# Optimization experiments

Measured on AMD Instinct MI355X. Metric: run time of the kernel, lower is better.

## Reference

```python
import jax, jax.numpy as jnp
import numpy as np

N_NODES = 100000
N_EDGES = 300000
D = 128
HID = 128

def setup_inputs() -> dict:
    key = jax.random.key(0)
    ks = jax.random.split(key, 12)
    s = lambda fan_in: 1.0 / np.sqrt(fan_in)
    return {
        "user_emb": jax.random.normal(ks[0], (N_NODES, D), jnp.float32),
        "item_emb": jax.random.normal(ks[1], (N_NODES, D), jnp.float32),
        "ei_ui": jax.random.randint(ks[2], (2, N_EDGES), 0, N_NODES, jnp.int64),
        "ei_iu": jax.random.randint(ks[3], (2, N_EDGES), 0, N_NODES, jnp.int64),
        "W_bi_ui": jax.random.normal(ks[4], (2 * D, HID), jnp.float32) * s(2 * D),
        "b_bi_ui": jnp.zeros((HID,), jnp.float32),
        "W1_ui": jax.random.normal(ks[5], (HID, HID), jnp.float32) * s(HID),
        "b1_ui": jnp.zeros((HID,), jnp.float32),
        "W2_ui": jax.random.normal(ks[6], (HID, 1), jnp.float32) * s(HID),
        "b2_ui": jnp.zeros((1,), jnp.float32),
        "W_bi_iu": jax.random.normal(ks[7], (2 * D, HID), jnp.float32) * s(2 * D),
        "b_bi_iu": jnp.zeros((HID,), jnp.float32),
        "W1_iu": jax.random.normal(ks[8], (HID, HID), jnp.float32) * s(HID),
        "b1_iu": jnp.zeros((HID,), jnp.float32),
        "W2_iu": jax.random.normal(ks[9], (HID, 1), jnp.float32) * s(HID),
        "b2_iu": jnp.zeros((1,), jnp.float32),
    }

def _decode_edge_type(src_emb, dst_emb, edge_index, W_bi, b_bi, W1, b1, W2, b2):
    # gather endpoint embeddings and concat -> [E, 2D]
    e = jnp.concatenate([src_emb[edge_index[0]], dst_emb[edge_index[1]]], axis=1)
    h = jax.nn.elu(e @ W_bi + b_bi)          # bilinear -> ELU
    h = jax.nn.elu(h @ W1 + b1)              # linear1 -> ELU
    p = jax.nn.sigmoid(h @ W2 + b2)          # linear2 -> sigmoid
    return p.reshape(-1)                     # [E]

def reference(user_emb, item_emb, ei_ui, ei_iu,
              W_bi_ui, b_bi_ui, W1_ui, b1_ui, W2_ui, b2_ui,
              W_bi_iu, b_bi_iu, W1_iu, b1_iu, W2_iu, b2_iu):
    # edge type (user, clicks, item): source=user, target=item
    p_ui = _decode_edge_type(user_emb, item_emb, ei_ui,
                             W_bi_ui, b_bi_ui, W1_ui, b1_ui, W2_ui, b2_ui)
    # edge type (item, clicked_by, user): source=item, target=user
    p_iu = _decode_edge_type(item_emb, user_emb, ei_iu,
                             W_bi_iu, b_bi_iu, W1_iu, b1_iu, W2_iu, b2_iu)
    return jnp.stack([p_ui, p_iu])  # [2, E]
```

## Files before the change

kernel.cpp:

```cpp
#include <hip/hip_runtime.h>

typedef __attribute__((ext_vector_type(8))) short short8;
typedef __attribute__((ext_vector_type(4))) float float4v;
typedef __attribute__((ext_vector_type(4))) int int4v;

#define E_EDGES 300000
#define EPB 128
#define NBLK ((E_EDGES + EPB - 1) / EPB)
#define TAB_ELEMS 12800000

__device__ __forceinline__ short f2bf(float f) {
    unsigned u = __float_as_uint(f);
    return (short)((u + 0x7FFFu + ((u >> 16) & 1u)) >> 16);
}
__device__ __forceinline__ unsigned pk_bf16(float a, float b) {
    unsigned ua = __float_as_uint(a), ub = __float_as_uint(b);
    ua += 0x7FFFu + ((ua >> 16) & 1u);
    ub += 0x7FFFu + ((ub >> 16) & 1u);
    return __builtin_amdgcn_perm(ub, ua, 0x07060302);
}
__device__ __forceinline__ void cp16(const void* g, void* l) {
    __builtin_amdgcn_global_load_lds(
        (const __attribute__((address_space(1))) unsigned int*)g,
        (__attribute__((address_space(3))) unsigned int*)l, 16, 0, 0);
}

__global__ void prep_all(const float* __restrict__ ue, const float* __restrict__ ie,
                         const float* __restrict__ Wbi_ui, const float* __restrict__ W1_ui,
                         const float* __restrict__ Wbi_iu, const float* __restrict__ W1_iu,
                         short* __restrict__ ws) {
    __shared__ short tr[64 * 68];
    const int t = blockIdx.y;
    const int tid = threadIdx.x;
    if (blockIdx.x < 1024) {
        const float* src = t ? ie : ue;
        short* dst = ws + 98304 + (size_t)t * TAB_ELEMS;
        const int stride = 1024 * 256;
        for (int g = blockIdx.x * 256 + tid; g < TAB_ELEMS / 8; g += stride) {
            const float* p = src + (size_t)g * 8;
            float4v v0 = ((const float4v*)p)[0];
            float4v v1 = ((const float4v*)p)[1];
            int4v w = { (int)pk_bf16(v0[0], v0[1]), (int)pk_bf16(v0[2], v0[3]),
                        (int)pk_bf16(v1[0], v1[1]), (int)pk_bf16(v1[2], v1[3]) };
            *(int4v*)(dst + (size_t)g * 8) = w;
        }
        return;
    }
    const int m = blockIdx.x - 1024;
    const float* W; int k0, n0, obase;
    if (m < 8) {
        int kt = m >> 1, nh = m & 1;
        W = t ? Wbi_iu : Wbi_ui; k0 = kt * 64; n0 = nh * 64;
        obase = t * 32768 + kt * 8192;
    } else {
        int mm = m - 8; int kt = mm >> 1, nh = mm & 1;
        W = t ? W1_iu : W1_ui; k0 = kt * 64; n0 = nh * 64;
        obase = 65536 + t * 16384 + kt * 8192;
    }
    for (int it = 0; it < 16; ++it) {
        int flat = it * 256 + tid;
        int kk = flat >> 6, nn = flat & 63;
        tr[nn * 68 + kk] = f2bf(W[(size_t)(k0 + kk) * 128 + n0 + nn]);
    }
    __syncthreads();
    for (int it = 0; it < 16; ++it) {
        int flat = it * 256 + tid;
        int nn = flat >> 6, kk = flat & 63;
        int n = n0 + nn;
        ws[obase + n * 64 + (kk ^ ((n & 7) << 3))] = tr[nn * 68 + kk];
    }
}

template<bool BF16G>
__launch_bounds__(256, 4)
__global__ void edge_decoder(
    const float* __restrict__ user_emb, const float* __restrict__ item_emb,
    const int* __restrict__ ei_ui, const int* __restrict__ ei_iu,
    const float* __restrict__ b_bi_ui, const float* __restrict__ b1_ui,
    const float* __restrict__ W2_ui, const float* __restrict__ b2_ui,
    const float* __restrict__ b_bi_iu, const float* __restrict__ b1_iu,
    const float* __restrict__ W2_iu, const float* __restrict__ b2_iu,
    const short* __restrict__ ws, const short* __restrict__ tab,
    float* __restrict__ out)
{
    __shared__ short Blds[128 * 64];
    __shared__ short Hlds[4 * 16 * 136];

    const int type = blockIdx.y;
    const int e0 = blockIdx.x * EPB;
    const int tid = threadIdx.x;
    const int wave = tid >> 6, lane = tid & 63;
    const int q = lane >> 4, ln = lane & 15;

    const int*   ei   = type ? ei_iu : ei_ui;
    const float* bbi  = type ? b_bi_iu : b_bi_ui;
    const float* b1v  = type ? b1_iu : b1_ui;
    const float* W2v  = type ? W2_iu : W2_ui;
    const float* b2v  = type ? b2_iu : b2_ui;
    const short* WbiT = ws + type * 32768;
    const short* W1T  = ws + 65536 + type * 16384;

    for (int c = 0; c < 4; ++c)
        cp16(WbiT + c * 2048 + tid * 8, Blds + c * 2048 + tid * 8);

    short8 a[2][8];
    if (BF16G) {
        for (int mt = 0; mt < 2; ++mt) {
            int erow = e0 + wave * 32 + mt * 16 + ln;
            int safe = (erow < E_EDGES) ? erow : 0;
            const short* sp = tab + (size_t)(type ? TAB_ELEMS : 0) + (size_t)ei[safe] * 128;
            const short* dp = tab + (size_t)(type ? 0 : TAB_ELEMS) + (size_t)ei[E_EDGES + safe] * 128;
            for (int ks = 0; ks < 4; ++ks)
                a[mt][ks] = *(const short8*)(sp + ks * 32 + q * 8);
            for (int ks = 4; ks < 8; ++ks)
                a[mt][ks] = *(const short8*)(dp + (ks - 4) * 32 + q * 8);
        }
    } else {
        const float* srcT = type ? item_emb : user_emb;
        const float* dstT = type ? user_emb : item_emb;
        for (int mt = 0; mt < 2; ++mt) {
            int erow = e0 + wave * 32 + mt * 16 + ln;
            int safe = (erow < E_EDGES) ? erow : 0;
            int si = ei[safe], di = ei[E_EDGES + safe];
            for (int ks = 0; ks < 8; ++ks) {
                const float* p = (ks < 4) ? (srcT + (size_t)si * 128 + ks * 32 + q * 8)
                                          : (dstT + (size_t)di * 128 + (ks - 4) * 32 + q * 8);
                float4v v0 = ((const float4v*)p)[0];
                float4v v1 = ((const float4v*)p)[1];
                int4v w = { (int)pk_bf16(v0[0], v0[1]), (int)pk_bf16(v0[2], v0[3]),
                            (int)pk_bf16(v1[0], v1[1]), (int)pk_bf16(v1[2], v1[3]) };
                a[mt][ks] = *(short8*)&w;
            }
        }
    }

    float4v acc[2][8];
    for (int nt = 0; nt < 8; ++nt) {
        float bb = bbi[nt * 16 + ln];
        acc[0][nt] = (float4v){bb, bb, bb, bb};
        acc[1][nt] = acc[0][nt];
    }

    const int swz = (ln & 7) << 3;

    for (int kt = 0; kt < 4; ++kt) {
        __syncthreads();
        for (int ks2 = 0; ks2 < 2; ++ks2) {
            int ka = (ks2 * 32 + q * 8) ^ swz;
            int ks = kt * 2 + ks2;
            for (int nt = 0; nt < 8; ++nt) {
                short8 bf = *(const short8*)&Blds[(nt * 16 + ln) * 64 + ka];
                acc[0][nt] = __builtin_amdgcn_mfma_f32_16x16x32_bf16(a[0][ks], bf, acc[0][nt], 0, 0, 0);
                acc[1][nt] = __builtin_amdgcn_mfma_f32_16x16x32_bf16(a[1][ks], bf, acc[1][nt], 0, 0, 0);
            }
        }
        __syncthreads();
        const short* nxt = (kt < 3) ? (WbiT + (kt + 1) * 8192) : W1T;
        for (int c = 0; c < 4; ++c)
            cp16(nxt + c * 2048 + tid * 8, Blds + c * 2048 + tid * 8);
    }

    short* Hw = Hlds + wave * (16 * 136);
    short8 a2[2][4];
    for (int mt = 0; mt < 2; ++mt) {
        for (int nt = 0; nt < 8; ++nt) {
            int col = nt * 16 + ln;
            float4v v = acc[mt][nt];
            for (int r = 0; r < 4; ++r) {
                float x = v[r];
                float h = x > 0.f ? x : (__expf(x) - 1.f);
                Hw[(q * 4 + r) * 136 + col] = f2bf(h);
            }
        }
        for (int ks = 0; ks < 4; ++ks)
            a2[mt][ks] = *(const short8*)&Hw[ln * 136 + ks * 32 + q * 8];
    }

    for (int nt = 0; nt < 8; ++nt) {
        float bb = b1v[nt * 16 + ln];
        acc[0][nt] = (float4v){bb, bb, bb, bb};
        acc[1][nt] = acc[0][nt];
    }

    for (int kt = 0; kt < 2; ++kt) {
        __syncthreads();
        for (int ks2 = 0; ks2 < 2; ++ks2) {
            int ka = (ks2 * 32 + q * 8) ^ swz;
            int ks = kt * 2 + ks2;
            for (int nt = 0; nt < 8; ++nt) {
                short8 bf = *(const short8*)&Blds[(nt * 16 + ln) * 64 + ka];
                acc[0][nt] = __builtin_amdgcn_mfma_f32_16x16x32_bf16(a2[0][ks], bf, acc[0][nt], 0, 0, 0);
                acc[1][nt] = __builtin_amdgcn_mfma_f32_16x16x32_bf16(a2[1][ks], bf, acc[1][nt], 0, 0, 0);
            }
        }
        __syncthreads();
        if (kt == 0)
            for (int c = 0; c < 4; ++c)
                cp16(W1T + 8192 + c * 2048 + tid * 8, Blds + c * 2048 + tid * 8);
    }

    for (int mt = 0; mt < 2; ++mt) {
        float s0 = 0.f, s1 = 0.f, s2 = 0.f, s3 = 0.f;
        for (int nt = 0; nt < 8; ++nt) {
            float wv = W2v[nt * 16 + ln];
            float4v v = acc[mt][nt];
            float x;
            x = v[0]; x = x > 0.f ? x : (__expf(x) - 1.f); s0 += x * wv;
            x = v[1]; x = x > 0.f ? x : (__expf(x) - 1.f); s1 += x * wv;
            x = v[2]; x = x > 0.f ? x : (__expf(x) - 1.f); s2 += x * wv;
            x = v[3]; x = x > 0.f ? x : (__expf(x) - 1.f); s3 += x * wv;
        }
        for (int off = 1; off < 16; off <<= 1) {
            s0 += __shfl_xor(s0, off);
            s1 += __shfl_xor(s1, off);
            s2 += __shfl_xor(s2, off);
            s3 += __shfl_xor(s3, off);
        }
        if (ln < 4) {
            float sv = (ln == 0) ? s0 : (ln == 1) ? s1 : (ln == 2) ? s2 : s3;
            int e = e0 + wave * 32 + mt * 16 + q * 4 + ln;
            if (e < E_EDGES) {
                float z = sv + b2v[0];
                out[type * E_EDGES + e] = 1.f / (1.f + __expf(-z));
            }
        }
    }
}

extern "C" void kernel_launch(void* const* d_in, const int* in_sizes, int n_in,
                              void* d_out, int out_size, void* d_ws, size_t ws_size,
                              hipStream_t stream) {
    const float* user_emb = (const float*)d_in[0];
    const float* item_emb = (const float*)d_in[1];
    const int*   ei_ui    = (const int*)d_in[2];
    const int*   ei_iu    = (const int*)d_in[3];
    const float* W_bi_ui  = (const float*)d_in[4];
    const float* b_bi_ui  = (const float*)d_in[5];
    const float* W1_ui    = (const float*)d_in[6];
    const float* b1_ui    = (const float*)d_in[7];
    const float* W2_ui    = (const float*)d_in[8];
    const float* b2_ui    = (const float*)d_in[9];
    const float* W_bi_iu  = (const float*)d_in[10];
    const float* b_bi_iu  = (const float*)d_in[11];
    const float* W1_iu    = (const float*)d_in[12];
    const float* b1_iu    = (const float*)d_in[13];
    const float* W2_iu    = (const float*)d_in[14];
    const float* b2_iu    = (const float*)d_in[15];
    short* ws  = (short*)d_ws;
    short* tab = ws + 98304;
    float* out = (float*)d_out;

    const size_t need = 98304u * 2u + (size_t)2 * TAB_ELEMS * 2u;

    hipLaunchKernelGGL(prep_all, dim3(1036, 2), dim3(256), 0, stream,
                       user_emb, item_emb, W_bi_ui, W1_ui, W_bi_iu, W1_iu, ws);
    if (ws_size >= need) {
        edge_decoder<true><<<dim3(NBLK, 2), dim3(256), 0, stream>>>(
            user_emb, item_emb, ei_ui, ei_iu,
            b_bi_ui, b1_ui, W2_ui, b2_ui,
            b_bi_iu, b1_iu, W2_iu, b2_iu,
            ws, tab, out);
    } else {
        edge_decoder<false><<<dim3(NBLK, 2), dim3(256), 0, stream>>>(
            user_emb, item_emb, ei_ui, ei_iu,
            b_bi_ui, b1_ui, W2_ui, b2_ui,
            b_bi_iu, b1_iu, W2_iu, b2_iu,
            ws, tab, out);
    }
}
```

Before: 272.4 us.

## Stage weights in 128-wide K chunks to halve LDS barrier rounds

Doubles the shared-memory weight tile from 64 to 128 K-columns and re-lays out the pre-transposed bf16 weights to a 128-stride swizzled format. The bilinear GEMM now runs in two staging rounds instead of four and the second GEMM in one instead of two, removing several syncthreads and cp16 reload phases. The larger LDS footprint lowers the occupancy hint from 4 to 3 blocks per CU, which may reduce latency hiding for the gather loads.

```diff
diff --git a/kernel.cpp b/kernel.cpp
--- a/kernel.cpp
+++ b/kernel.cpp
@@ -47,15 +47,17 @@
         return;
     }
     const int m = blockIdx.x - 1024;
-    const float* W; int k0, n0, obase;
+    const float* W; int k0, n0, obase, kbase;
     if (m < 8) {
         int kt = m >> 1, nh = m & 1;
         W = t ? Wbi_iu : Wbi_ui; k0 = kt * 64; n0 = nh * 64;
-        obase = t * 32768 + kt * 8192;
+        obase = t * 32768 + (kt >> 1) * 16384;
+        kbase = (kt & 1) * 64;
     } else {
         int mm = m - 8; int kt = mm >> 1, nh = mm & 1;
         W = t ? W1_iu : W1_ui; k0 = kt * 64; n0 = nh * 64;
-        obase = 65536 + t * 16384 + kt * 8192;
+        obase = 65536 + t * 16384;
+        kbase = kt * 64;
     }
     for (int it = 0; it < 16; ++it) {
         int flat = it * 256 + tid;
@@ -67,12 +69,15 @@
         int flat = it * 256 + tid;
         int nn = flat >> 6, kk = flat & 63;
         int n = n0 + nn;
-        ws[obase + n * 64 + (kk ^ ((n & 7) << 3))] = tr[nn * 68 + kk];
+        int kkst = kbase + kk;
+        int c = kkst >> 3, co = kkst & 7;
+        int p = (c & 8) | ((c ^ (n & 7)) & 7);
+        ws[obase + n * 128 + p * 8 + co] = tr[nn * 68 + kk];
     }
 }
 
 template<bool BF16G>
-__launch_bounds__(256, 4)
+__launch_bounds__(256, 3)
 __global__ void edge_decoder(
     const float* __restrict__ user_emb, const float* __restrict__ item_emb,
     const int* __restrict__ ei_ui, const int* __restrict__ ei_iu,
@@ -83,7 +88,7 @@
     const short* __restrict__ ws, const short* __restrict__ tab,
     float* __restrict__ out)
 {
-    __shared__ short Blds[128 * 64];
+    __shared__ short Blds[128 * 128];
     __shared__ short Hlds[4 * 16 * 136];
 
     const int type = blockIdx.y;
@@ -100,7 +105,7 @@
     const short* WbiT = ws + type * 32768;
     const short* W1T  = ws + 65536 + type * 16384;
 
-    for (int c = 0; c < 4; ++c)
+    for (int c = 0; c < 8; ++c)
         cp16(WbiT + c * 2048 + tid * 8, Blds + c * 2048 + tid * 8);
 
     short8 a[2][8];
@@ -141,24 +146,34 @@
         acc[1][nt] = acc[0][nt];
     }
 
-    const int swz = (ln & 7) << 3;
-
-    for (int kt = 0; kt < 4; ++kt) {
-        __syncthreads();
-        for (int ks2 = 0; ks2 < 2; ++ks2) {
-            int ka = (ks2 * 32 + q * 8) ^ swz;
-            int ks = kt * 2 + ks2;
-            for (int nt = 0; nt < 8; ++nt) {
-                short8 bf = *(const short8*)&Blds[(nt * 16 + ln) * 64 + ka];
-                acc[0][nt] = __builtin_amdgcn_mfma_f32_16x16x32_bf16(a[0][ks], bf, acc[0][nt], 0, 0, 0);
-                acc[1][nt] = __builtin_amdgcn_mfma_f32_16x16x32_bf16(a[1][ks], bf, acc[1][nt], 0, 0, 0);
-            }
-        }
-        __syncthreads();
-        const short* nxt = (kt < 3) ? (WbiT + (kt + 1) * 8192) : W1T;
-        for (int c = 0; c < 4; ++c)
-            cp16(nxt + c * 2048 + tid * 8, Blds + c * 2048 + tid * 8);
-    }
+    const int swz7 = ln & 7;
+#define KAOF(ks2) ((((((ks2) * 4 + q) & 8) | ((((ks2) * 4 + q) ^ swz7) & 7))) * 8)
+
+    __syncthreads();
+    for (int ks2 = 0; ks2 < 4; ++ks2) {
+        int ka = KAOF(ks2);
+        for (int nt = 0; nt < 8; ++nt) {
+            short8 bf = *(const short8*)&Blds[(nt * 16 + ln) * 128 + ka];
+            acc[0][nt] = __builtin_amdgcn_mfma_f32_16x16x32_bf16(a[0][ks2], bf, acc[0][nt], 0, 0, 0);
+            acc[1][nt] = __builtin_amdgcn_mfma_f32_16x16x32_bf16(a[1][ks2], bf, acc[1][nt], 0, 0, 0);
+        }
+    }
+    __syncthreads();
+    for (int c = 0; c < 8; ++c)
+        cp16(WbiT + 16384 + c * 2048 + tid * 8, Blds + c * 2048 + tid * 8);
+
+    __syncthreads();
+    for (int ks2 = 0; ks2 < 4; ++ks2) {
+        int ka = KAOF(ks2);
+        for (int nt = 0; nt < 8; ++nt) {
+            short8 bf = *(const short8*)&Blds[(nt * 16 + ln) * 128 + ka];
+            acc[0][nt] = __builtin_amdgcn_mfma_f32_16x16x32_bf16(a[0][4 + ks2], bf, acc[0][nt], 0, 0, 0);
+            acc[1][nt] = __builtin_amdgcn_mfma_f32_16x16x32_bf16(a[1][4 + ks2], bf, acc[1][nt], 0, 0, 0);
+        }
+    }
+    __syncthreads();
+    for (int c = 0; c < 8; ++c)
+        cp16(W1T + c * 2048 + tid * 8, Blds + c * 2048 + tid * 8);
 
     short* Hw = Hlds + wave * (16 * 136);
     short8 a2[2][4];
@@ -182,22 +197,16 @@
         acc[1][nt] = acc[0][nt];
     }
 
-    for (int kt = 0; kt < 2; ++kt) {
-        __syncthreads();
-        for (int ks2 = 0; ks2 < 2; ++ks2) {
-            int ka = (ks2 * 32 + q * 8) ^ swz;
-            int ks = kt * 2 + ks2;
-            for (int nt = 0; nt < 8; ++nt) {
-                short8 bf = *(const short8*)&Blds[(nt * 16 + ln) * 64 + ka];
-                acc[0][nt] = __builtin_amdgcn_mfma_f32_16x16x32_bf16(a2[0][ks], bf, acc[0][nt], 0, 0, 0);
-                acc[1][nt] = __builtin_amdgcn_mfma_f32_16x16x32_bf16(a2[1][ks], bf, acc[1][nt], 0, 0, 0);
-            }
-        }
-        __syncthreads();
-        if (kt == 0)
-            for (int c = 0; c < 4; ++c)
-                cp16(W1T + 8192 + c * 2048 + tid * 8, Blds + c * 2048 + tid * 8);
-    }
+    __syncthreads();
+    for (int ks2 = 0; ks2 < 4; ++ks2) {
+        int ka = KAOF(ks2);
+        for (int nt = 0; nt < 8; ++nt) {
+            short8 bf = *(const short8*)&Blds[(nt * 16 + ln) * 128 + ka];
+            acc[0][nt] = __builtin_amdgcn_mfma_f32_16x16x32_bf16(a2[0][ks2], bf, acc[0][nt], 0, 0, 0);
+            acc[1][nt] = __builtin_amdgcn_mfma_f32_16x16x32_bf16(a2[1][ks2], bf, acc[1][nt], 0, 0, 0);
+        }
+    }
+#undef KAOF
 
     for (int mt = 0; mt < 2; ++mt) {
         float s0 = 0.f, s1 = 0.f, s2 = 0.f, s3 = 0.f;
```

Measured after the change: 250.8 us. -7.9%, faster.
